# Kernel tuning notes

Measured on AMD Instinct MI355X. Metric: run time of the kernel, lower is better.

Reference implementation:

```python
import jax, jax.numpy as jnp
import numpy as np

T, B = 512, 256
OBS, FEAT, H, ACT = 128, 512, 256, 16
LOG2PI = float(np.log(2.0 * np.pi))


def layer_norm(x, w, b, eps=1e-5):
    m = x.mean(-1, keepdims=True)
    v = ((x - m) ** 2).mean(-1, keepdims=True)
    return (x - m) / jnp.sqrt(v + eps) * w + b


def mlp_features(x, W1, b1, W2, b2, gw, gb):
    h = jax.nn.relu(x @ W1.T + b1)
    h = layer_norm(h @ W2.T + b2, gw, gb)
    return jax.nn.relu(h)


def masked_lstm_scan(feat, done, h0, c0, Wih, Whh, bih, bhh):
    # feat: [T,B,H], done: [T,B] float, h0/c0: [B,H]. PyTorch gate order i,f,g,o.
    def step(carry, inp):
        h, c = carry
        x, d = inp
        m = (1.0 - d)[:, None]
        h = h * m
        c = c * m
        g = x @ Wih.T + bih + h @ Whh.T + bhh
        i, f, gg, o = jnp.split(g, 4, axis=-1)
        c = jax.nn.sigmoid(f) * c + jax.nn.sigmoid(i) * jnp.tanh(gg)
        h = jax.nn.sigmoid(o) * jnp.tanh(c)
        return (h, c), h
    (hT, cT), hs = jax.lax.scan(step, (h0, c0), (feat, done))
    return hs, hT, cT


def setup_inputs():
    key = jax.random.key(0)
    ks = jax.random.split(key, 40)
    rn = lambda k, s, sc=0.05: jax.random.normal(k, s, dtype=jnp.float32) * sc
    inp = {}
    inp["x"] = jax.random.normal(ks[0], (T * B, OBS), dtype=jnp.float32)
    inp["done"] = jax.random.randint(ks[1], (T * B,), 0, 2).astype(jnp.int32)
    inp["actor_h0"] = rn(ks[2], (1, B, H), 0.1)
    inp["actor_c0"] = rn(ks[3], (1, B, H), 0.1)
    inp["critic_h0"] = rn(ks[4], (1, B, H), 0.1)
    inp["critic_c0"] = rn(ks[5], (1, B, H), 0.1)
    inp["action"] = jax.random.normal(ks[6], (T * B, ACT), dtype=jnp.float32)
    j = 7
    for p in ("a", "c"):
        inp[p + "_W1"] = rn(ks[j], (FEAT, OBS)); j += 1
        inp[p + "_b1"] = jnp.zeros((FEAT,), jnp.float32)
        inp[p + "_W2"] = rn(ks[j], (H, FEAT)); j += 1
        inp[p + "_b2"] = jnp.zeros((H,), jnp.float32)
        inp[p + "_flnw"] = jnp.ones((H,), jnp.float32)
        inp[p + "_flnb"] = jnp.zeros((H,), jnp.float32)
        inp[p + "_Wih"] = rn(ks[j], (4 * H, H)); j += 1
        inp[p + "_Whh"] = rn(ks[j], (4 * H, H)); j += 1
        inp[p + "_bih"] = jnp.zeros((4 * H,), jnp.float32)
        inp[p + "_bhh"] = jnp.zeros((4 * H,), jnp.float32)
        inp[p + "_lnw"] = jnp.ones((H,), jnp.float32)
        inp[p + "_lnb"] = jnp.zeros((H,), jnp.float32)
    inp["a_mW"] = rn(ks[j], (ACT, H)); j += 1
    inp["a_mb"] = jnp.zeros((ACT,), jnp.float32)
    inp["a_logstd"] = jnp.zeros((1, ACT), jnp.float32)
    inp["c_hW"] = rn(ks[j], (1, H)); j += 1
    inp["c_hb"] = jnp.zeros((1,), jnp.float32)
    return inp


def reference(x, done, actor_h0, actor_c0, critic_h0, critic_c0, action,
              a_W1, a_b1, a_W2, a_b2, a_flnw, a_flnb, a_Wih, a_Whh, a_bih, a_bhh,
              a_lnw, a_lnb, a_mW, a_mb, a_logstd,
              c_W1, c_b1, c_W2, c_b2, c_flnw, c_flnb, c_Wih, c_Whh, c_bih, c_bhh,
              c_lnw, c_lnb, c_hW, c_hb):
    Bn = actor_h0.shape[1]
    N = x.shape[0]
    Tn = N // Bn
    d = done.astype(jnp.float32).reshape(Tn, Bn)
    # actor branch
    a_feat = mlp_features(x, a_W1, a_b1, a_W2, a_b2, a_flnw, a_flnb).reshape(Tn, Bn, -1)
    hs, ah, acell = masked_lstm_scan(a_feat, d, actor_h0[0], actor_c0[0], a_Wih, a_Whh, a_bih, a_bhh)
    ha = layer_norm(hs.reshape(N, -1), a_lnw, a_lnb)
    mean = ha @ a_mW.T + a_mb
    logstd = jnp.broadcast_to(a_logstd, mean.shape)
    std = jnp.exp(logstd)
    logprob = (-0.5 * ((action - mean) / std) ** 2 - logstd - 0.5 * LOG2PI).sum(1)
    entropy = (0.5 + 0.5 * LOG2PI + logstd).sum(1)
    # critic branch
    c_feat = mlp_features(x, c_W1, c_b1, c_W2, c_b2, c_flnw, c_flnb).reshape(Tn, Bn, -1)
    cs, ch, ccell = masked_lstm_scan(c_feat, d, critic_h0[0], critic_c0[0], c_Wih, c_Whh, c_bih, c_bhh)
    hc = layer_norm(cs.reshape(N, -1), c_lnw, c_lnb)
    value = hc @ c_hW.T + c_hb
    return (logprob, entropy, value, ah[None], acell[None], ch[None], ccell[None])
```

## Files before the change

### kernel.cpp

```cpp
#include <hip/hip_runtime.h>

typedef unsigned short u16;
typedef unsigned long long u64;
typedef __attribute__((ext_vector_type(8))) short short8;
typedef __attribute__((ext_vector_type(4))) float floatx4;
typedef __attribute__((ext_vector_type(4))) float f32x4;
typedef __attribute__((ext_vector_type(4))) int intx4;

#define LOG2PI_F 1.8378770664093453f
#define LOG2E_F 1.4426950408889634f
#define TWOLOG2E_F 2.8853900817779268f

__device__ inline float bf2f(u16 u) { return __uint_as_float(((unsigned)u) << 16); }
__device__ inline u16 f2bf(float f) {
  unsigned u = __float_as_uint(f);
  u += 0x7fff + ((u >> 16) & 1);
  return (u16)(u >> 16);
}

struct PrepArgs {
  const float* src[18];
  const float* src2[18];
  void* dst[18];
  int mode[18];
  int n[18];
  int blk0[19];
  int nseg;
};

__global__ __launch_bounds__(256) void k_prep(PrepArgs a) {
  int b = blockIdx.x, s = 0;
  while (s + 1 < a.nseg && b >= a.blk0[s + 1]) ++s;
  int i = (b - a.blk0[s]) * 1024 + threadIdx.x * 4;
  if (i >= a.n[s]) return;
  if (a.mode[s] == 0) {
    f32x4 v = *(const f32x4*)(a.src[s] + i);
    u64 p = (u64)f2bf(v[0]) | ((u64)f2bf(v[1]) << 16)
          | ((u64)f2bf(v[2]) << 32) | ((u64)f2bf(v[3]) << 48);
    *(u64*)((u16*)a.dst[s] + i) = p;
  } else if (a.mode[s] == 1) {
    f32x4 x = *(const f32x4*)(a.src[s] + i);
    f32x4 y = *(const f32x4*)(a.src2[s] + i);
    *(f32x4*)((float*)a.dst[s] + i) = x + y;
  } else {
    *(f32x4*)((float*)a.dst[s] + i) = *(const f32x4*)(a.src[s] + i);
  }
}

__global__ __launch_bounds__(256) void k_quant(const float* __restrict__ w0,
                                               const float* __restrict__ w1,
                                               char* __restrict__ q, float* __restrict__ sr) {
  int tid = threadIdx.x, lane = tid & 63;
  int row = blockIdx.x * 4 + (tid >> 6);
  int br = row >> 10, r = row & 1023;
  const float* src = (br ? w1 : w0) + (size_t)r * 256 + lane * 4;
  f32x4 v = *(const f32x4*)src;
  float m = fmaxf(fmaxf(fabsf(v[0]), fabsf(v[1])), fmaxf(fabsf(v[2]), fabsf(v[3])));
#pragma unroll
  for (int o = 32; o >= 1; o >>= 1) m = fmaxf(m, __shfl_xor(m, o));
  float inv = m > 0.f ? 127.f / m : 0.f;
  int pk = 0;
#pragma unroll
  for (int c = 0; c < 4; ++c) {
    int qq = __float2int_rn(v[c] * inv);
    qq = qq > 127 ? 127 : (qq < -127 ? -127 : qq);
    pk |= (qq & 255) << (8 * c);
  }
  *(int*)(q + (size_t)row * 256 + lane * 4) = pk;
  if (lane == 0) {
    float sf = (r >= 512 && r < 768) ? TWOLOG2E_F : -LOG2E_F;
    sr[row] = m * (1.f / (127.f * 127.f)) * sf;
  }
}

template <int EPI, int AF32>
__global__ __launch_bounds__(256, 2) void k_gemm(
    const void* __restrict__ Agv, const u16* __restrict__ Wg,
    const float* __restrict__ biasP, void* __restrict__ outv,
    int Nn, int K, int relu, int Tseg,
    long az, long wz, long oz) {
  __shared__ u16 As[128][72];
  __shared__ u16 Ws[128][72];
  const int tid = threadIdx.x;
  const int z = blockIdx.z;
  const int bn = blockIdx.x * 128;
  const int bm = blockIdx.y * 128;
  const int w = tid >> 6, lane = tid & 63, lm = lane & 15, lq = lane >> 4;
  const int wr = (w >> 1) * 64, wc = (w & 1) * 64;
  const int tr = tid >> 3, tc = (tid & 7) * 8;

  const u16* Ab = (const u16*)Agv;
  const float* Af = (const float*)Agv;
  const u16* Wb = Wg + (size_t)z * wz;

  floatx4 acc[4][4] = {};

  for (int k0 = 0; k0 < K; k0 += 64) {
    __syncthreads();
#pragma unroll
    for (int rr = 0; rr < 4; ++rr) {
      int row = rr * 32 + tr;
      if (AF32) {
        const float* src = Af + (size_t)z * az + (size_t)(bm + row) * K + k0 + tc;
        f32x4 v0 = *(const f32x4*)src;
        f32x4 v1 = *(const f32x4*)(src + 4);
        short8 sv;
#pragma unroll
        for (int c = 0; c < 4; ++c) { sv[c] = (short)f2bf(v0[c]); sv[4 + c] = (short)f2bf(v1[c]); }
        *(short8*)&As[row][tc] = sv;
      } else {
        *(short8*)&As[row][tc] = *(const short8*)(Ab + (size_t)z * az + (size_t)(bm + row) * K + k0 + tc);
      }
      *(short8*)&Ws[row][tc] = *(const short8*)(Wb + (size_t)(bn + row) * K + k0 + tc);
    }
    __syncthreads();
#pragma unroll
    for (int kk = 0; kk < 2; ++kk) {
      short8 a4[4], b4[4];
#pragma unroll
      for (int i = 0; i < 4; ++i) {
        a4[i] = *(const short8*)&As[wr + i * 16 + lm][kk * 32 + lq * 8];
        b4[i] = *(const short8*)&Ws[wc + i * 16 + lm][kk * 32 + lq * 8];
      }
#pragma unroll
      for (int i = 0; i < 4; ++i)
#pragma unroll
        for (int j = 0; j < 4; ++j)
          acc[i][j] = __builtin_amdgcn_mfma_f32_16x16x32_bf16(a4[i], b4[j], acc[i][j], 0, 0, 0);
    }
  }

#pragma unroll
  for (int i = 0; i < 4; ++i) {
#pragma unroll
    for (int j = 0; j < 4; ++j) {
      int col = bn + wc + j * 16 + lm;
      float bv = biasP[(size_t)z * Nn + col];
      float v[4];
#pragma unroll
      for (int r = 0; r < 4; ++r) {
        float t = acc[i][j][r] + bv;
        v[r] = relu ? fmaxf(t, 0.f) : t;
      }
      int row0l = bm + wr + i * 16 + lq * 4;
      if (EPI == 1) {
        u16* o = (u16*)outv + (size_t)z * oz;
#pragma unroll
        for (int r = 0; r < 4; ++r) o[(size_t)(row0l + r) * Nn + col] = f2bf(v[r]);
      } else {
        float s = (col >= 512 && col < 768) ? TWOLOG2E_F : -LOG2E_F;
        int t_l = row0l >> 8;
        int bfull = row0l & 255;
        int bbx = bfull >> 4;
        int mq = (bfull >> 2) & 3;
        u64 p = (u64)f2bf(v[0] * s) | ((u64)f2bf(v[1] * s) << 16)
              | ((u64)f2bf(v[2] * s) << 32) | ((u64)f2bf(v[3] * s) << 48);
        u16* o = (u16*)outv + (size_t)z * oz;
        size_t idx = ((((size_t)bbx * Tseg + t_l) * 4 + mq) * 1024 + col) * 4;
        *(u64*)(o + idx) = p;
      }
    }
  }
}

__global__ __launch_bounds__(256) void k_ln_relu(const u16* __restrict__ in,
                                                 const float* __restrict__ lnp,
                                                 u16* __restrict__ out,
                                                 long inz, long outz) {
  int z = blockIdx.y;
  int w = threadIdx.x >> 6, lane = threadIdx.x & 63;
  size_t row = (size_t)blockIdx.x * 4 + w;
  const u16* ip = in + (size_t)z * inz;
  u16* op = out + (size_t)z * outz;
  const float* gw = lnp + (size_t)z * 512;
  const float* gb = gw + 256;
  u64 hv = *(const u64*)(ip + row * 256 + lane * 4);
  float x[4];
#pragma unroll
  for (int c = 0; c < 4; ++c) x[c] = bf2f((u16)(hv >> (16 * c)));
  float s = x[0] + x[1] + x[2] + x[3];
  float q = x[0] * x[0] + x[1] * x[1] + x[2] * x[2] + x[3] * x[3];
#pragma unroll
  for (int o = 32; o >= 1; o >>= 1) { s += __shfl_xor(s, o); q += __shfl_xor(q, o); }
  float mean = s * (1.f / 256.f);
  float var = q * (1.f / 256.f) - mean * mean;
  float rs = rsqrtf(var + 1e-5f);
  u64 p = 0;
#pragma unroll
  for (int c = 0; c < 4; ++c) {
    int k = lane * 4 + c;
    float y = (x[c] - mean) * rs * gw[k] + gb[k];
    y = fmaxf(y, 0.f);
    p |= ((u64)f2bf(y)) << (16 * c);
  }
  *(u64*)(op + row * 256 + lane * 4) = p;
}

struct ScanArgs {
  const u16 *gin0, *gin1;
  const char *whq0, *whq1;
  const float *sr0, *sr1;
  const float *h00, *h01, *c00, *c01;
  char *hs0, *hs1;
  float *hsv0, *hsv1, *csv0, *csv1;
  const int* done;
  int t0, Tseg;
};

template <int LDSW>
__global__ __launch_bounds__(512, 2) void k_scan(ScanArgs A) {
  const int bb = blockIdx.x & 31, br = blockIdx.x >> 5;
  const int bbx = bb >> 1, half = bb & 1;
  const int rb = bb << 3;
  const int tid = threadIdx.x;
  const int w = tid >> 6, lane = tid & 63, lm = lane & 15, lq = lane >> 4;
  const int u = lq >> 1;
  const int jj = (w + 8 * u) * 16 + lm;
  const int rlo = (lq & 1) * 4;
  const int wj = w + 8 * u;
  const int hoff = (wj >> 2) * 1024 + ((wj & 3) * 16 + rlo) * 16 + lm;

  extern __shared__ char dsm[];
  char* wl = dsm;
  char* hl = dsm + (LDSW ? 131072 : 0);

  const char* whq = br ? A.whq1 : A.whq0;
  const float* srP = br ? A.sr1 : A.sr0;
  const u16* gin = (br ? A.gin1 : A.gin0) + (size_t)bbx * A.Tseg * 16384;
  const float* h0 = br ? A.h01 : A.h00;
  const float* c0 = br ? A.c01 : A.c00;
  char* hs = (br ? A.hs1 : A.hs0) + bbx * 4096;
  float* hsv = br ? A.hsv1 : A.hsv0;
  float* csv = br ? A.csv1 : A.csv0;

  intx4 wreg[4][4];
#pragma unroll
  for (int a = 0; a < 4; ++a)
#pragma unroll
    for (int kk = 0; kk < 4; ++kk)
      wreg[a][kk] = *(const intx4*)(whq + (size_t)((w + 8 * a) * 16 + lm) * 256 + kk * 64 + lq * 16);

  if (LDSW) {
#pragma unroll
    for (int t = 0; t < 4; ++t)
#pragma unroll
      for (int kk = 0; kk < 4; ++kk) {
        intx4 v = *(const intx4*)(whq + (size_t)((w + 8 * (4 + t)) * 16 + lm) * 256 + kk * 64 + lq * 16);
        *(intx4*)&wl[(size_t)w * 16384 + t * 4096 + kk * 1024 + lane * 16] = v;
      }
  }

  float srw[4];
#pragma unroll
  for (int g = 0; g < 4; ++g) srw[g] = srP[g * 256 + jj];

  float creg[4];
#pragma unroll
  for (int r = 0; r < 4; ++r)
    creg[r] = c0[(size_t)(rb + rlo + r) * 256 + jj];

  {
    int c = tid & 255, buf = tid >> 8;
    int kk = c >> 6, lqk = (c >> 4) & 3, m = c & 15;
    intx4 val = {0, 0, 0, 0};
    if (buf == 0 && m < 8) {
      const float* hp = h0 + (size_t)(rb + m) * 256 + kk * 64 + lqk * 16;
#pragma unroll
      for (int q4 = 0; q4 < 4; ++q4) {
        int pk = 0;
#pragma unroll
        for (int b = 0; b < 4; ++b) {
          int qv = __float2int_rn(hp[q4 * 4 + b] * 127.f);
          qv = qv > 127 ? 127 : (qv < -127 ? -127 : qv);
          pk |= (qv & 255) << (8 * b);
        }
        val[q4] = pk;
      }
    }
    *(intx4*)&hl[buf * 4096 + c * 16] = val;
  }
  __syncthreads();

  const int mq = half * 2 + (lq & 1);
  u64 ghold[4];
#pragma unroll
  for (int g = 0; g < 4; ++g)
    ghold[g] = *(const u64*)(gin + ((size_t)mq * 1024 + g * 256 + jj) * 4);
  int daN = A.done[(size_t)A.t0 * 256 + rb + (lm & 7)];
  intx4 dcN = *(const intx4*)(A.done + (size_t)A.t0 * 256 + rb + rlo);

  intx4 z4 = {0, 0, 0, 0};

  for (int tl = 0; tl < A.Tseg; ++tl) {
    const int curo = (tl & 1) * 4096, nxto = curo ^ 4096;

    floatx4 gf[4];
#pragma unroll
    for (int g = 0; g < 4; ++g) {
      u64 gv = ghold[g];
      floatx4 v;
      v[0] = bf2f((u16)gv); v[1] = bf2f((u16)(gv >> 16));
      v[2] = bf2f((u16)(gv >> 32)); v[3] = bf2f((u16)(gv >> 48));
      gf[g] = v;
    }
    int da = daN;
    intx4 dc = dcN;

    if (tl + 1 < A.Tseg) {
#pragma unroll
      for (int g = 0; g < 4; ++g)
        ghold[g] = *(const u64*)(gin + (((size_t)(tl + 1) * 4 + mq) * 1024 + g * 256 + jj) * 4);
      int tn = A.t0 + tl + 1;
      daN = A.done[(size_t)tn * 256 + rb + (lm & 7)];
      dcN = *(const intx4*)(A.done + (size_t)tn * 256 + rb + rlo);
    }

    intx4 af[4];
#pragma unroll
    for (int kk = 0; kk < 4; ++kk) {
      intx4 hv = *(const intx4*)&hl[curo + kk * 1024 + lane * 16];
      af[kk] = da ? z4 : hv;
    }

    intx4 acc[8] = {};
#pragma unroll
    for (int kk = 0; kk < 4; ++kk)
#pragma unroll
      for (int a = 0; a < 4; ++a)
        acc[a] = __builtin_amdgcn_mfma_i32_16x16x64_i8(af[kk], wreg[a][kk], acc[a], 0, 0, 0);
    if (LDSW) {
#pragma unroll
      for (int t = 0; t < 4; ++t)
#pragma unroll
        for (int kk = 0; kk < 4; ++kk) {
          intx4 wv = *(const intx4*)&wl[(size_t)w * 16384 + t * 4096 + kk * 1024 + lane * 16];
          acc[4 + t] = __builtin_amdgcn_mfma_i32_16x16x64_i8(af[kk], wv, acc[4 + t], 0, 0, 0);
        }
    } else {
#pragma unroll
      for (int t = 0; t < 4; ++t)
#pragma unroll
        for (int kk = 0; kk < 4; ++kk) {
          intx4 wv = *(const intx4*)(whq + (size_t)((w + 8 * (4 + t)) * 16 + lm) * 256 + kk * 64 + lq * 16);
          acc[4 + t] = __builtin_amdgcn_mfma_i32_16x16x64_i8(af[kk], wv, acc[4 + t], 0, 0, 0);
        }
    }

    float av[4][4];
#pragma unroll
    for (int g = 0; g < 4; ++g)
#pragma unroll
      for (int r = 0; r < 4; ++r) {
        int oth = __shfl_xor(acc[2 * g + 1][r], 32);
        av[g][r] = (float)(lq < 2 ? acc[2 * g][r] : oth);
      }

#pragma unroll
    for (int r = 0; r < 4; ++r) {
      float cprev = dc[r] ? 0.f : creg[r];
      float xi = fmaf(av[0][r], srw[0], gf[0][r]);
      float xf = fmaf(av[1][r], srw[1], gf[1][r]);
      float xg = fmaf(av[2][r], srw[2], gf[2][r]);
      float xo = fmaf(av[3][r], srw[3], gf[3][r]);
      float ig = __builtin_amdgcn_rcpf(1.f + __builtin_amdgcn_exp2f(xi));
      float fg = __builtin_amdgcn_rcpf(1.f + __builtin_amdgcn_exp2f(xf));
      float gg = 1.f - 2.f * __builtin_amdgcn_rcpf(1.f + __builtin_amdgcn_exp2f(xg));
      float og = __builtin_amdgcn_rcpf(1.f + __builtin_amdgcn_exp2f(xo));
      float cn = fg * cprev + ig * gg;
      creg[r] = cn;
      float th = 1.f - 2.f * __builtin_amdgcn_rcpf(1.f + __builtin_amdgcn_exp2f(TWOLOG2E_F * cn));
      float hn = og * th;
      int qv = __float2int_rn(hn * 127.f);
      hl[nxto + hoff + r * 16] = (char)qv;
      if (tl == A.Tseg - 1) {
        size_t idx = (size_t)(rb + rlo + r) * 256 + jj;
        hsv[idx] = hn;
        csv[idx] = cn;
      }
    }
    asm volatile("s_waitcnt lgkmcnt(0)" ::: "memory");
    __builtin_amdgcn_s_barrier();
    __builtin_amdgcn_sched_barrier(0);
    {
      int idx = tid * 4;
      int kk2 = idx >> 9, i2 = idx & 511;
      int lqk2 = i2 >> 7, m2 = (i2 >> 4) & 7, b2 = i2 & 15;
      int lo = nxto + kk2 * 1024 + lqk2 * 256 + m2 * 16 + b2;
      int go = kk2 * 1024 + lqk2 * 256 + half * 128 + m2 * 16 + b2;
      *(int*)(hs + (size_t)tl * 65536 + go) = *(const int*)&hl[lo];
    }
  }
}

__global__ __launch_bounds__(256) void k_head(
    const char* __restrict__ hs_a, const char* __restrict__ hs_c,
    const float* __restrict__ a_lnw, const float* __restrict__ a_lnb,
    const float* __restrict__ c_lnw, const float* __restrict__ c_lnb,
    const float* __restrict__ mW, const float* __restrict__ mb,
    const float* __restrict__ logstd, const float* __restrict__ hW,
    const float* __restrict__ hb, const float* __restrict__ action,
    float* __restrict__ lp, float* __restrict__ ent, float* __restrict__ val,
    int row0) {
  __shared__ float smW[16][260];
  __shared__ float shW[256];
  __shared__ float spar[4][256];
  __shared__ float hrow[4][264];
  int tid = threadIdx.x;
  for (int i = tid; i < 4096; i += 256) smW[i >> 8][i & 255] = mW[i];
  shW[tid] = hW[tid];
  spar[0][tid] = a_lnw[tid]; spar[1][tid] = a_lnb[tid];
  spar[2][tid] = c_lnw[tid]; spar[3][tid] = c_lnb[tid];
  __syncthreads();

  int w = tid >> 6, lane = tid & 63, lm = lane & 15, lq = lane >> 4;
  float entc = 0.f;
#pragma unroll
  for (int j = 0; j < 16; ++j) entc += 0.5f + 0.5f * LOG2PI_F + logstd[j];
  float ls = logstd[lm];
  float sd = __expf(ls);
  float mbj = mb[lm];

  int rbase = (blockIdx.x * 4 + w) * 16;
  for (int rr = 0; rr < 16; ++rr) {
    int row = rbase + rr;
    int m = row & 15;
    size_t base = (size_t)(row >> 8) * 65536 + (size_t)((row >> 4) & 15) * 4096;
    int off = (lane >> 4) * 1024 + (m + 16 * ((lane >> 2) & 3)) * 16 + (lane & 3) * 4;
    int va = *(const int*)(hs_a + base + off);
    float x[4];
#pragma unroll
    for (int c = 0; c < 4; ++c) x[c] = (float)((va << (24 - 8 * c)) >> 24) * (1.f / 127.f);
    float s = x[0] + x[1] + x[2] + x[3];
    float q = x[0] * x[0] + x[1] * x[1] + x[2] * x[2] + x[3] * x[3];
#pragma unroll
    for (int o = 32; o >= 1; o >>= 1) { s += __shfl_xor(s, o); q += __shfl_xor(q, o); }
    float mean = s * (1.f / 256.f);
    float rs = rsqrtf(q * (1.f / 256.f) - mean * mean + 1e-5f);
    floatx4 hh;
#pragma unroll
    for (int c = 0; c < 4; ++c) {
      int k = lane * 4 + c;
      hh[c] = (x[c] - mean) * rs * spar[0][k] + spar[1][k];
    }
    *(floatx4*)&hrow[w][lane * 4] = hh;
    float p = 0.f;
#pragma unroll 16
    for (int k2 = 0; k2 < 64; ++k2) {
      int kx = lq * 64 + ((k2 + lq * 16) & 63);
      p = fmaf(hrow[w][kx], smW[lm][kx], p);
    }
    p += __shfl_xor(p, 16);
    p += __shfl_xor(p, 32);
    float meanj = p + mbj;
    float aj = action[(size_t)(row0 + row) * 16 + lm];
    float z = (aj - meanj) / sd;
    float term = -0.5f * z * z - ls - 0.5f * LOG2PI_F;
    term += __shfl_xor(term, 1);
    term += __shfl_xor(term, 2);
    term += __shfl_xor(term, 4);
    term += __shfl_xor(term, 8);
    int vc = *(const int*)(hs_c + base + off);
    float y[4];
#pragma unroll
    for (int c = 0; c < 4; ++c) y[c] = (float)((vc << (24 - 8 * c)) >> 24) * (1.f / 127.f);
    float s2 = y[0] + y[1] + y[2] + y[3];
    float q2 = y[0] * y[0] + y[1] * y[1] + y[2] * y[2] + y[3] * y[3];
#pragma unroll
    for (int o = 32; o >= 1; o >>= 1) { s2 += __shfl_xor(s2, o); q2 += __shfl_xor(q2, o); }
    float mean2 = s2 * (1.f / 256.f);
    float rs2 = rsqrtf(q2 * (1.f / 256.f) - mean2 * mean2 + 1e-5f);
    float pv = 0.f;
#pragma unroll
    for (int c = 0; c < 4; ++c) {
      int k = lane * 4 + c;
      float hc = (y[c] - mean2) * rs2 * spar[2][k] + spar[3][k];
      pv = fmaf(hc, shW[k], pv);
    }
#pragma unroll
    for (int o = 32; o >= 1; o >>= 1) pv += __shfl_xor(pv, o);
    if (lane == 0) {
      lp[row0 + row] = term;
      ent[row0 + row] = entc;
      val[row0 + row] = pv + hb[0];
    }
  }
}

extern "C" void kernel_launch(void* const* d_in, const int* in_sizes, int n_in,
                              void* d_out, int out_size, void* d_ws, size_t ws_size,
                              hipStream_t stream) {
  const int N = 131072, T = 512;
  const float* x = (const float*)d_in[0];
  const int* done = (const int*)d_in[1];
  const float* h0i[2] = {(const float*)d_in[2], (const float*)d_in[4]};
  const float* c0i[2] = {(const float*)d_in[3], (const float*)d_in[5]};
  const float* action = (const float*)d_in[6];
  const float *W1[2], *b1[2], *W2[2], *b2[2], *flnw[2], *flnb[2];
  const float *Wih[2], *Whh[2], *bih[2], *bhh[2], *lnw[2], *lnb[2];
  for (int br = 0; br < 2; ++br) {
    int o = 7 + br * 12;
    W1[br] = (const float*)d_in[o + 0];  b1[br] = (const float*)d_in[o + 1];
    W2[br] = (const float*)d_in[o + 2];  b2[br] = (const float*)d_in[o + 3];
    flnw[br] = (const float*)d_in[o + 4]; flnb[br] = (const float*)d_in[o + 5];
    Wih[br] = (const float*)d_in[o + 6]; Whh[br] = (const float*)d_in[o + 7];
    bih[br] = (const float*)d_in[o + 8]; bhh[br] = (const float*)d_in[o + 9];
    lnw[br] = (const float*)d_in[o + 10]; lnb[br] = (const float*)d_in[o + 11];
  }
  const float* mW = (const float*)d_in[31];
  const float* mb = (const float*)d_in[32];
  const float* logstd = (const float*)d_in[33];
  const float* hW = (const float*)d_in[34];
  const float* hb = (const float*)d_in[35];

  float* out = (float*)d_out;
  float* o_lp = out;
  float* o_ent = out + N;
  float* o_val = out + 2 * N;
  float* o_ah = out + 3 * N;
  float* o_ac = o_ah + 65536;
  float* o_ch = o_ac + 65536;
  float* o_cc = o_ch + 65536;

  auto rq = [&](long sr2, long st2) -> size_t {
    long Ts = T / st2, Ms = N / sr2;
    size_t s = 0;
    auto al = [&](size_t b) { s += (b + 255) & ~(size_t)255; };
    al(2 * 65536 * 2); al(2 * 131072 * 2); al(2 * 262144 * 2);
    al(2 * 262144); al(2048 * 4);
    al(2 * 1024 * 4); al(2 * 512 * 4); al(2 * 256 * 4); al(1024 * 4);
    al(2 * 65536 * 4); al(2 * 65536 * 4);
    al((size_t)2 * Ms * 512 * 2);
    al((size_t)2 * Ms * 256 * 2);
    al((size_t)2 * N * 256 * 2);
    al((size_t)2 * Ts * 262144 * 2);
    al((size_t)2 * Ts * 65536);
    return s;
  };
  int sr = 16, st = 16;
  const int cand[7][2] = {{1, 1}, {2, 2}, {4, 4}, {4, 8}, {8, 8}, {8, 16}, {16, 16}};
  for (int i = 0; i < 7; ++i)
    if (rq(cand[i][0], cand[i][1]) + ((size_t)4 << 20) <= ws_size) { sr = cand[i][0]; st = cand[i][1]; break; }
  const long Ts = T / st, Ms = N / sr;

  char* pp = (char*)d_ws;
  auto carve = [&](size_t b) -> void* { void* r = pp; pp += (b + 255) & ~(size_t)255; return r; };
  u16* W1b = (u16*)carve(2 * 65536 * 2);
  u16* W2b = (u16*)carve(2 * 131072 * 2);
  u16* Wihb = (u16*)carve(2 * 262144 * 2);
  char* whhq = (char*)carve(2 * 262144);
  float* srowP = (float*)carve(2048 * 4);
  float* bihh = (float*)carve(2 * 1024 * 4);
  float* b1c = (float*)carve(2 * 512 * 4);
  float* b2c = (float*)carve(2 * 256 * 4);
  float* lnp = (float*)carve(1024 * 4);
  float* hsv = (float*)carve(2 * 65536 * 4);
  float* csv = (float*)carve(2 * 65536 * 4);
  u16* h1 = (u16*)carve((size_t)2 * Ms * 512 * 2);
  u16* g2 = (u16*)carve((size_t)2 * Ms * 256 * 2);
  u16* featP = (u16*)carve((size_t)2 * N * 256 * 2);
  u16* ginP = (u16*)carve((size_t)2 * Ts * 262144 * 2);
  char* hsbP = (char*)carve((size_t)2 * Ts * 65536);

  PrepArgs pa{};
  int ns = 0, blk = 0;
  auto addseg = [&](const float* s1, const float* s2, void* d, int n, int mode) {
    pa.src[ns] = s1; pa.src2[ns] = s2; pa.dst[ns] = d; pa.mode[ns] = mode; pa.n[ns] = n;
    pa.blk0[ns] = blk; blk += (n + 1023) / 1024; ++ns;
  };
  for (int br = 0; br < 2; ++br) {
    addseg(W1[br], nullptr, W1b + br * 65536, 65536, 0);
    addseg(W2[br], nullptr, W2b + br * 131072, 131072, 0);
    addseg(Wih[br], nullptr, Wihb + br * 262144, 262144, 0);
    addseg(bih[br], bhh[br], bihh + br * 1024, 1024, 1);
    addseg(b1[br], nullptr, b1c + br * 512, 512, 2);
    addseg(b2[br], nullptr, b2c + br * 256, 256, 2);
    addseg(flnw[br], nullptr, lnp + br * 512, 256, 2);
    addseg(flnb[br], nullptr, lnp + br * 512 + 256, 256, 2);
  }
  pa.nseg = ns;
  pa.blk0[ns] = blk;
  k_prep<<<blk, 256, 0, stream>>>(pa);
  k_quant<<<512, 256, 0, stream>>>(Whh[0], Whh[1], whhq, srowP);

  int ldsw = 1;
  if (hipFuncSetAttribute((const void*)&k_scan<1>, hipFuncAttributeMaxDynamicSharedMemorySize,
                          139264) != hipSuccess)
    ldsw = 0;

  for (int s = 0; s < sr; ++s) {
    k_gemm<1, 1><<<dim3(4, Ms / 128, 2), 256, 0, stream>>>(
        x + (size_t)s * Ms * 128, W1b, b1c, h1, 512, 128, 1, 0,
        0L, 65536L, (long)Ms * 512);
    k_gemm<1, 0><<<dim3(2, Ms / 128, 2), 256, 0, stream>>>(
        h1, W2b, b2c, g2, 256, 512, 0, 0,
        (long)Ms * 512, 131072L, (long)Ms * 256);
    k_ln_relu<<<dim3(Ms / 4, 2), 256, 0, stream>>>(
        g2, lnp, featP + (size_t)s * Ms * 256, (long)Ms * 256, (long)N * 256);
  }

  for (int s = 0; s < st; ++s) {
    long t0 = s * Ts;
    k_gemm<2, 0><<<dim3(8, Ts * 2, 2), 256, 0, stream>>>(
        featP + (size_t)t0 * 65536, Wihb, bihh, ginP, 1024, 256, 0, (int)Ts,
        (long)N * 256, 262144L, Ts * 262144L);
    ScanArgs sa;
    sa.gin0 = ginP; sa.gin1 = ginP + Ts * 262144;
    sa.whq0 = whhq; sa.whq1 = whhq + 262144;
    sa.sr0 = srowP; sa.sr1 = srowP + 1024;
    sa.h00 = s ? hsv : h0i[0]; sa.h01 = s ? hsv + 65536 : h0i[1];
    sa.c00 = s ? csv : c0i[0]; sa.c01 = s ? csv + 65536 : c0i[1];
    sa.hs0 = hsbP; sa.hs1 = hsbP + Ts * 65536;
    bool last = (s == st - 1);
    sa.hsv0 = last ? o_ah : hsv; sa.hsv1 = last ? o_ch : hsv + 65536;
    sa.csv0 = last ? o_ac : csv; sa.csv1 = last ? o_cc : csv + 65536;
    sa.done = done; sa.t0 = (int)t0; sa.Tseg = (int)Ts;
    if (ldsw) k_scan<1><<<64, 512, 139264, stream>>>(sa);
    else      k_scan<0><<<64, 512, 8192, stream>>>(sa);
    k_head<<<(int)(Ts * 256 / 64), 256, 0, stream>>>(
        hsbP, hsbP + Ts * 65536, lnw[0], lnb[0], lnw[1], lnb[1],
        mW, mb, logstd, hW, hb, action,
        o_lp, o_ent, o_val, (int)(t0 * 256));
  }
}
```

Measured before the change: 2.156 ms.

## Hold all recurrent weights in registers instead of staging half in LDS

The scan kernel now keeps the full int8 Whh slice (8x4 intx4 per lane) in registers and drops the LDS weight copy and its per-step LDS reads. The bf16 gate-input decode is also moved after the MFMA block so it can overlap with matrix work. This removes 128 KB of LDS traffic per timestep on the serial recurrence path. In exchange it doubles the weight register footprint, which under launch_bounds(512,2) risks spills or pressure on the accumulators.

After: 2.078 ms. -3.6%, faster.

```diff
diff --git a/kernel.cpp b/kernel.cpp
--- a/kernel.cpp
+++ b/kernel.cpp
@@ -207,7 +207,6 @@
   int t0, Tseg;
 };
 
-template <int LDSW>
 __global__ __launch_bounds__(512, 2) void k_scan(ScanArgs A) {
   const int bb = blockIdx.x & 31, br = blockIdx.x >> 5;
   const int bbx = bb >> 1, half = bb & 1;
@@ -221,8 +220,7 @@
   const int hoff = (wj >> 2) * 1024 + ((wj & 3) * 16 + rlo) * 16 + lm;
 
   extern __shared__ char dsm[];
-  char* wl = dsm;
-  char* hl = dsm + (LDSW ? 131072 : 0);
+  char* hl = dsm;
 
   const char* whq = br ? A.whq1 : A.whq0;
   const float* srP = br ? A.sr1 : A.sr0;
@@ -233,22 +231,12 @@
   float* hsv = br ? A.hsv1 : A.hsv0;
   float* csv = br ? A.csv1 : A.csv0;
 
-  intx4 wreg[4][4];
-#pragma unroll
-  for (int a = 0; a < 4; ++a)
+  intx4 wreg[8][4];
+#pragma unroll
+  for (int a = 0; a < 8; ++a)
 #pragma unroll
     for (int kk = 0; kk < 4; ++kk)
       wreg[a][kk] = *(const intx4*)(whq + (size_t)((w + 8 * a) * 16 + lm) * 256 + kk * 64 + lq * 16);
-
-  if (LDSW) {
-#pragma unroll
-    for (int t = 0; t < 4; ++t)
-#pragma unroll
-      for (int kk = 0; kk < 4; ++kk) {
-        intx4 v = *(const intx4*)(whq + (size_t)((w + 8 * (4 + t)) * 16 + lm) * 256 + kk * 64 + lq * 16);
-        *(intx4*)&wl[(size_t)w * 16384 + t * 4096 + kk * 1024 + lane * 16] = v;
-      }
-  }
 
   float srw[4];
 #pragma unroll
@@ -282,10 +270,10 @@
   __syncthreads();
 
   const int mq = half * 2 + (lq & 1);
-  u64 ghold[4];
+  u64 gnxt[4];
 #pragma unroll
   for (int g = 0; g < 4; ++g)
-    ghold[g] = *(const u64*)(gin + ((size_t)mq * 1024 + g * 256 + jj) * 4);
+    gnxt[g] = *(const u64*)(gin + ((size_t)mq * 1024 + g * 256 + jj) * 4);
   int daN = A.done[(size_t)A.t0 * 256 + rb + (lm & 7)];
   intx4 dcN = *(const intx4*)(A.done + (size_t)A.t0 * 256 + rb + rlo);
 
@@ -294,66 +282,53 @@
   for (int tl = 0; tl < A.Tseg; ++tl) {
     const int curo = (tl & 1) * 4096, nxto = curo ^ 4096;
 
+    u64 gcur[4];
+#pragma unroll
+    for (int g = 0; g < 4; ++g) gcur[g] = gnxt[g];
+    int da = daN;
+    intx4 dc = dcN;
+
+    if (tl + 1 < A.Tseg) {
+#pragma unroll
+      for (int g = 0; g < 4; ++g)
+        gnxt[g] = *(const u64*)(gin + (((size_t)(tl + 1) * 4 + mq) * 1024 + g * 256 + jj) * 4);
+      int tn = A.t0 + tl + 1;
+      daN = A.done[(size_t)tn * 256 + rb + (lm & 7)];
+      dcN = *(const intx4*)(A.done + (size_t)tn * 256 + rb + rlo);
+    }
+
+    intx4 af[4];
+#pragma unroll
+    for (int kk = 0; kk < 4; ++kk) {
+      intx4 hv = *(const intx4*)&hl[curo + kk * 1024 + lane * 16];
+      af[kk] = da ? z4 : hv;
+    }
+
+    intx4 acc[8] = {};
+#pragma unroll
+    for (int kk = 0; kk < 4; ++kk)
+#pragma unroll
+      for (int a = 0; a < 8; ++a)
+        acc[a] = __builtin_amdgcn_mfma_i32_16x16x64_i8(af[kk], wreg[a][kk], acc[a], 0, 0, 0);
+
+    float av[4][4];
+#pragma unroll
+    for (int g = 0; g < 4; ++g)
+#pragma unroll
+      for (int r = 0; r < 4; ++r) {
+        int oth = __shfl_xor(acc[2 * g + 1][r], 32);
+        av[g][r] = (float)(lq < 2 ? acc[2 * g][r] : oth);
+      }
+
     floatx4 gf[4];
 #pragma unroll
     for (int g = 0; g < 4; ++g) {
-      u64 gv = ghold[g];
+      u64 gv = gcur[g];
       floatx4 v;
       v[0] = bf2f((u16)gv); v[1] = bf2f((u16)(gv >> 16));
       v[2] = bf2f((u16)(gv >> 32)); v[3] = bf2f((u16)(gv >> 48));
       gf[g] = v;
     }
-    int da = daN;
-    intx4 dc = dcN;
-
-    if (tl + 1 < A.Tseg) {
-#pragma unroll
-      for (int g = 0; g < 4; ++g)
-        ghold[g] = *(const u64*)(gin + (((size_t)(tl + 1) * 4 + mq) * 1024 + g * 256 + jj) * 4);
-      int tn = A.t0 + tl + 1;
-      daN = A.done[(size_t)tn * 256 + rb + (lm & 7)];
-      dcN = *(const intx4*)(A.done + (size_t)tn * 256 + rb + rlo);
-    }
-
-    intx4 af[4];
-#pragma unroll
-    for (int kk = 0; kk < 4; ++kk) {
-      intx4 hv = *(const intx4*)&hl[curo + kk * 1024 + lane * 16];
-      af[kk] = da ? z4 : hv;
-    }
-
-    intx4 acc[8] = {};
-#pragma unroll
-    for (int kk = 0; kk < 4; ++kk)
-#pragma unroll
-      for (int a = 0; a < 4; ++a)
-        acc[a] = __builtin_amdgcn_mfma_i32_16x16x64_i8(af[kk], wreg[a][kk], acc[a], 0, 0, 0);
-    if (LDSW) {
-#pragma unroll
-      for (int t = 0; t < 4; ++t)
-#pragma unroll
-        for (int kk = 0; kk < 4; ++kk) {
-          intx4 wv = *(const intx4*)&wl[(size_t)w * 16384 + t * 4096 + kk * 1024 + lane * 16];
-          acc[4 + t] = __builtin_amdgcn_mfma_i32_16x16x64_i8(af[kk], wv, acc[4 + t], 0, 0, 0);
-        }
-    } else {
-#pragma unroll
-      for (int t = 0; t < 4; ++t)
-#pragma unroll
-        for (int kk = 0; kk < 4; ++kk) {
-          intx4 wv = *(const intx4*)(whq + (size_t)((w + 8 * (4 + t)) * 16 + lm) * 256 + kk * 64 + lq * 16);
-          acc[4 + t] = __builtin_amdgcn_mfma_i32_16x16x64_i8(af[kk], wv, acc[4 + t], 0, 0, 0);
-        }
-    }
-
-    float av[4][4];
-#pragma unroll
-    for (int g = 0; g < 4; ++g)
-#pragma unroll
-      for (int r = 0; r < 4; ++r) {
-        int oth = __shfl_xor(acc[2 * g + 1][r], 32);
-        av[g][r] = (float)(lq < 2 ? acc[2 * g][r] : oth);
-      }
 
 #pragma unroll
     for (int r = 0; r < 4; ++r) {
@@ -582,11 +557,6 @@
   k_prep<<<blk, 256, 0, stream>>>(pa);
   k_quant<<<512, 256, 0, stream>>>(Whh[0], Whh[1], whhq, srowP);
 
-  int ldsw = 1;
-  if (hipFuncSetAttribute((const void*)&k_scan<1>, hipFuncAttributeMaxDynamicSharedMemorySize,
-                          139264) != hipSuccess)
-    ldsw = 0;
-
   for (int s = 0; s < sr; ++s) {
     k_gemm<1, 1><<<dim3(4, Ms / 128, 2), 256, 0, stream>>>(
         x + (size_t)s * Ms * 128, W1b, b1c, h1, 512, 128, 1, 0,
@@ -614,8 +584,7 @@
     sa.hsv0 = last ? o_ah : hsv; sa.hsv1 = last ? o_ch : hsv + 65536;
     sa.csv0 = last ? o_ac : csv; sa.csv1 = last ? o_cc : csv + 65536;
     sa.done = done; sa.t0 = (int)t0; sa.Tseg = (int)Ts;
-    if (ldsw) k_scan<1><<<64, 512, 139264, stream>>>(sa);
-    else      k_scan<0><<<64, 512, 8192, stream>>>(sa);
+    k_scan<<<64, 512, 8192, stream>>>(sa);
     k_head<<<(int)(Ts * 256 / 64), 256, 0, stream>>>(
         hsbP, hsbP + Ts * 65536, lnw[0], lnb[0], lnw[1], lnb[1],
         mW, mb, logstd, hW, hb, action,
```
